# Performance work log

Measured on AMD Instinct MI355X. Metric: run time of the kernel, lower is better.

## Reference

```python
import jax, jax.numpy as jnp
import numpy as np

IN_F, OUT_F = 4096, 16384
B, S = 4, 2048
SCALE = 0.02

def setup_inputs() -> dict:
    key = jax.random.key(0)
    k1, k2 = jax.random.split(key)
    x = jax.random.normal(k1, (B, S, IN_F), dtype=jnp.float32)
    # ternary weights in {-1, 0, +1}
    weight_ternary = jax.random.randint(k2, (OUT_F, IN_F), -1, 2, dtype=jnp.int32)
    weight_scale = jnp.full((1,), SCALE, dtype=jnp.float32)
    return {"x": x, "weight_ternary": weight_ternary, "weight_scale": weight_scale}

def reference(x, weight_ternary, weight_scale):
    # dequantize ternary weight
    w = weight_ternary.astype(jnp.float32) * weight_scale  # [OUT_F, IN_F]
    # per-token int8 activation quant/dequant
    x_scale = jnp.clip(jnp.max(jnp.abs(x), axis=-1, keepdims=True), 1e-5, None)
    x_quant = jnp.round(jnp.clip(x / x_scale * 127.0, -128.0, 127.0))
    x_final = x_quant * x_scale / 127.0
    # linear: x_final @ w.T
    return jnp.einsum('bsi,oi->bso', x_final, w)
```

## Files before the change

kernel.cpp:

```cpp
#include <hip/hip_runtime.h>

#define IN_F 4096
#define OUT_F 16384
#define MTOK 8192

#define BM 256
#define BN 256
#define BK 64
#define NKT (IN_F / BK)

typedef __attribute__((ext_vector_type(4)))  int   i32x4;
typedef __attribute__((ext_vector_type(4)))  float f32x4;

__device__ __forceinline__ void gload_lds16(const void* g, void* l) {
    __builtin_amdgcn_global_load_lds(
        (const __attribute__((address_space(1))) void*)g,
        (__attribute__((address_space(3))) void*)l,
        16, 0, 0);
}

__global__ __launch_bounds__(256) void k_quant(const float* __restrict__ x,
                                               char* __restrict__ xq,
                                               float* __restrict__ xs) {
    const int m = blockIdx.x;
    const int t = threadIdx.x;
    const float* xrow = x + (size_t)m * IN_F;

    f32x4 v[4];
    float mx = 0.f;
#pragma unroll
    for (int i = 0; i < 4; ++i) {
        v[i] = *(const f32x4*)&xrow[(i * 256 + t) * 4];
        mx = fmaxf(mx, fmaxf(fmaxf(fabsf(v[i].x), fabsf(v[i].y)),
                             fmaxf(fabsf(v[i].z), fabsf(v[i].w))));
    }
#pragma unroll
    for (int off = 32; off > 0; off >>= 1)
        mx = fmaxf(mx, __shfl_xor(mx, off));

    __shared__ float wmax[4];
    const int wid = t >> 6;
    if ((t & 63) == 0) wmax[wid] = mx;
    __syncthreads();
    const float scale = fmaxf(fmaxf(fmaxf(wmax[0], wmax[1]),
                                    fmaxf(wmax[2], wmax[3])), 1e-5f);
    const float inv = 127.0f / scale;

    int* xqi = (int*)(xq + (size_t)m * IN_F);
#pragma unroll
    for (int i = 0; i < 4; ++i) {
        int q0 = (int)rintf(fminf(fmaxf(v[i].x * inv, -128.f), 127.f));
        int q1 = (int)rintf(fminf(fmaxf(v[i].y * inv, -128.f), 127.f));
        int q2 = (int)rintf(fminf(fmaxf(v[i].z * inv, -128.f), 127.f));
        int q3 = (int)rintf(fminf(fmaxf(v[i].w * inv, -128.f), 127.f));
        xqi[i * 256 + t] = (q0 & 255) | ((q1 & 255) << 8) |
                           ((q2 & 255) << 16) | (q3 << 24);
    }
    if (t == 0) xs[m] = scale;
}

__global__ __launch_bounds__(256) void k_wconv(const int* __restrict__ wt,
                                               int* __restrict__ w8) {
    const int total4 = OUT_F * IN_F / 4;
    int idx = blockIdx.x * 256 + threadIdx.x;
    const int stride = gridDim.x * 256;
    for (; idx < total4; idx += stride) {
        i32x4 w = *(const i32x4*)&wt[(size_t)idx * 4];
        w8[idx] = (w.x & 255) | ((w.y & 255) << 8) |
                  ((w.z & 255) << 16) | (w.w << 24);
    }
}

__global__ __launch_bounds__(512, 2) void k_gemm(
    const char*  __restrict__ Aq,
    const char*  __restrict__ Bq,
    const float* __restrict__ xs,
    const float* __restrict__ wsp,
    float*       __restrict__ C) {
    __shared__ __align__(16) char lds[98304];

    const int t    = threadIdx.x;
    const int lane = t & 63;
    const int wid  = t >> 6;
    const int wr   = wid >> 2;
    const int wc   = wid & 3;

    const int bid = blockIdx.x;
    const int bn  = (bid & 7) * 8 + ((bid >> 3) & 7);
    const int bm  = bid >> 6;
    const int mBase = bm * BM;
    const int nBase = bn * BN;

    const int r0 = t >> 2;
    const int c0 = (((t & 3) ^ ((t >> 3) & 3)) << 4);

#define STAGE(kt, bx) do {                                                     \
        const size_t ks = (size_t)(kt) * BK;                                   \
        gload_lds16(Aq + (size_t)(mBase + r0) * IN_F + ks + c0,                \
                    lds + (bx) * 16384 + wid * 1024);                          \
        gload_lds16(Aq + (size_t)(mBase + 128 + r0) * IN_F + ks + c0,          \
                    lds + (bx) * 16384 + 8192 + wid * 1024);                   \
        gload_lds16(Bq + (size_t)(nBase + r0) * IN_F + ks + c0,                \
                    lds + 49152 + (bx) * 16384 + wid * 1024);                  \
        gload_lds16(Bq + (size_t)(nBase + 128 + r0) * IN_F + ks + c0,          \
                    lds + 49152 + (bx) * 16384 + 8192 + wid * 1024);           \
    } while (0)

    const int fOff = (lane & 15) * 64 + ((((lane >> 4) ^ (lane >> 1)) & 3) << 4);
    const char* ldsA = lds + wr * 8192;
    const char* ldsB = lds + 49152 + wc * 4096;

#define BAR()   __builtin_amdgcn_s_barrier()
#define VM4()   asm volatile("s_waitcnt vmcnt(4)" ::: "memory")
#define VM0()   asm volatile("s_waitcnt vmcnt(0)" ::: "memory")

    i32x4 acc[8][4];
#pragma unroll
    for (int i = 0; i < 8; ++i)
#pragma unroll
        for (int j = 0; j < 4; ++j)
            acc[i][j] = (i32x4){0, 0, 0, 0};

    STAGE(0, 0);
    STAGE(1, 1);
    VM4();
    BAR();

    int x = 0, x2 = 2;
    for (int kt = 0; kt < NKT; ++kt) {
        const int xo = x * 16384;
        const bool more = (kt + 2 < NKT);

        i32x4 b[4], a[8];
#pragma unroll
        for (int ni = 0; ni < 4; ++ni)
            b[ni] = *(const i32x4*)(ldsB + xo + ni * 1024 + fOff);
#pragma unroll
        for (int mi = 0; mi < 8; ++mi)
            a[mi] = *(const i32x4*)(ldsA + xo + mi * 1024 + fOff);

        if (more) STAGE(kt + 2, x2);

        __builtin_amdgcn_s_setprio(1);
#pragma unroll
        for (int mi = 0; mi < 8; ++mi)
#pragma unroll
            for (int ni = 0; ni < 4; ++ni)
                acc[mi][ni] = __builtin_amdgcn_mfma_i32_16x16x64_i8(
                    a[mi], b[ni], acc[mi][ni], 0, 0, 0);
        __builtin_amdgcn_s_setprio(0);

        if (more) { VM4(); } else { VM0(); }
        BAR();

        x  = (x  == 2) ? 0 : x  + 1;
        x2 = (x2 == 2) ? 0 : x2 + 1;
    }

    const float wsc = wsp[0] * (1.0f / 127.0f);
#pragma unroll
    for (int mi = 0; mi < 8; ++mi) {
        float rs[4];
#pragma unroll
        for (int r = 0; r < 4; ++r)
            rs[r] = xs[mBase + wr * 128 + mi * 16 + (lane >> 4) * 4 + r] * wsc;
#pragma unroll
        for (int ni = 0; ni < 4; ++ni) {
            const int col = nBase + wc * 64 + ni * 16 + (lane & 15);
#pragma unroll
            for (int r = 0; r < 4; ++r) {
                const int row = mBase + wr * 128 + mi * 16 + (lane >> 4) * 4 + r;
                C[(size_t)row * OUT_F + col] = (float)acc[mi][ni][r] * rs[r];
            }
        }
    }
}

extern "C" void kernel_launch(void* const* d_in, const int* in_sizes, int n_in,
                              void* d_out, int out_size, void* d_ws, size_t ws_size,
                              hipStream_t stream) {
    const float* x   = (const float*)d_in[0];
    const int*   wt  = (const int*)d_in[1];
    const float* wsp = (const float*)d_in[2];
    float* out = (float*)d_out;

    char*  w8 = (char*)d_ws;
    char*  xq = (char*)d_ws + (size_t)OUT_F * IN_F;
    float* xs = (float*)((char*)d_ws + (size_t)OUT_F * IN_F
                                     + (size_t)MTOK * IN_F);

    k_wconv<<<8192, 256, 0, stream>>>(wt, (int*)w8);
    k_quant<<<MTOK, 256, 0, stream>>>(x, xq, xs);

    const int grid = (MTOK / BM) * (OUT_F / BN);
    k_gemm<<<grid, 512, 0, stream>>>(xq, w8, xs, wsp, out);
}
```

Measured before the change: 644.0 us.

## Load B fragments directly from global into registers, halving LDS usage

The weight (B) tile no longer goes through LDS. Each wave loads its B MFMA fragments straight from global memory into registers, double-buffered one k-step ahead, while A still uses the 3-stage LDS pipeline. LDS drops from 96KB to 48KB, which could allow more occupancy and removes the LDS reads for B. In exchange, B reuse across the two row-waves now happens in cache rather than LDS, so global traffic rises, and the loop is unrolled by two with a peeled tail and adjusted vmcnt waits.

Result: slower. 906.8 us (+40.8%).

```diff
diff --git a/kernel.cpp b/kernel.cpp
--- a/kernel.cpp
+++ b/kernel.cpp
@@ -77,7 +77,7 @@
     const float* __restrict__ xs,
     const float* __restrict__ wsp,
     float*       __restrict__ C) {
-    __shared__ __align__(16) char lds[98304];
+    __shared__ __align__(16) char lds[49152];
 
     const int t    = threadIdx.x;
     const int lane = t & 63;
@@ -100,19 +100,37 @@
                     lds + (bx) * 16384 + wid * 1024);                          \
         gload_lds16(Aq + (size_t)(mBase + 128 + r0) * IN_F + ks + c0,          \
                     lds + (bx) * 16384 + 8192 + wid * 1024);                   \
-        gload_lds16(Bq + (size_t)(nBase + r0) * IN_F + ks + c0,                \
-                    lds + 49152 + (bx) * 16384 + wid * 1024);                  \
-        gload_lds16(Bq + (size_t)(nBase + 128 + r0) * IN_F + ks + c0,          \
-                    lds + 49152 + (bx) * 16384 + 8192 + wid * 1024);           \
     } while (0)
 
     const int fOff = (lane & 15) * 64 + ((((lane >> 4) ^ (lane >> 1)) & 3) << 4);
     const char* ldsA = lds + wr * 8192;
-    const char* ldsB = lds + 49152 + wc * 4096;
+
+    const char* bBase = Bq + (size_t)(nBase + wc * 64 + (lane & 15)) * IN_F
+                           + ((lane >> 4) << 4);
+
+#define LOADB(dst, kt)                                                         \
+    _Pragma("unroll")                                                          \
+    for (int ni = 0; ni < 4; ++ni)                                             \
+        dst[ni] = *(const i32x4*)(bBase + ni * 65536 + (size_t)(kt) * BK);
+
+#define RDA(a, XO)                                                             \
+    _Pragma("unroll")                                                          \
+    for (int mi = 0; mi < 8; ++mi)                                             \
+        a[mi] = *(const i32x4*)(ldsA + (XO) + mi * 1024 + fOff);
+
+#define MFMAC(a, b)                                                            \
+    __builtin_amdgcn_s_setprio(1);                                             \
+    _Pragma("unroll")                                                          \
+    for (int mi = 0; mi < 8; ++mi)                                             \
+        _Pragma("unroll")                                                      \
+        for (int ni = 0; ni < 4; ++ni)                                         \
+            acc[mi][ni] = __builtin_amdgcn_mfma_i32_16x16x64_i8(               \
+                a[mi], b[ni], acc[mi][ni], 0, 0, 0);                           \
+    __builtin_amdgcn_s_setprio(0);
 
 #define BAR()   __builtin_amdgcn_s_barrier()
+#define VM6()   asm volatile("s_waitcnt vmcnt(6)" ::: "memory")
 #define VM4()   asm volatile("s_waitcnt vmcnt(4)" ::: "memory")
-#define VM0()   asm volatile("s_waitcnt vmcnt(0)" ::: "memory")
 
     i32x4 acc[8][4];
 #pragma unroll
@@ -121,40 +139,45 @@
         for (int j = 0; j < 4; ++j)
             acc[i][j] = (i32x4){0, 0, 0, 0};
 
+    i32x4 bA[4], bB[4];
+
     STAGE(0, 0);
     STAGE(1, 1);
-    VM4();
+    LOADB(bA, 0);
+    VM6();
     BAR();
 
     int x = 0, x2 = 2;
-    for (int kt = 0; kt < NKT; ++kt) {
-        const int xo = x * 16384;
-        const bool more = (kt + 2 < NKT);
-
-        i32x4 b[4], a[8];
-#pragma unroll
-        for (int ni = 0; ni < 4; ++ni)
-            b[ni] = *(const i32x4*)(ldsB + xo + ni * 1024 + fOff);
-#pragma unroll
-        for (int mi = 0; mi < 8; ++mi)
-            a[mi] = *(const i32x4*)(ldsA + xo + mi * 1024 + fOff);
-
-        if (more) STAGE(kt + 2, x2);
-
-        __builtin_amdgcn_s_setprio(1);
-#pragma unroll
-        for (int mi = 0; mi < 8; ++mi)
-#pragma unroll
-            for (int ni = 0; ni < 4; ++ni)
-                acc[mi][ni] = __builtin_amdgcn_mfma_i32_16x16x64_i8(
-                    a[mi], b[ni], acc[mi][ni], 0, 0, 0);
-        __builtin_amdgcn_s_setprio(0);
-
-        if (more) { VM4(); } else { VM0(); }
+#define GBODY(kt, BU, BL) do {                                                 \
+        LOADB(BL, (kt) + 1);                                                   \
+        i32x4 a[8];                                                            \
+        RDA(a, x * 16384);                                                     \
+        STAGE((kt) + 2, x2);                                                   \
+        MFMAC(a, BU);                                                          \
+        VM6();                                                                 \
+        BAR();                                                                 \
+        x  = (x  == 2) ? 0 : x  + 1;                                           \
+        x2 = (x2 == 2) ? 0 : x2 + 1;                                           \
+    } while (0)
+
+    for (int it = 0; it < 31; ++it) {
+        const int k0 = 2 * it;
+        GBODY(k0,     bA, bB);
+        GBODY(k0 + 1, bB, bA);
+    }
+
+    {
+        LOADB(bB, 63);
+        i32x4 a[8];
+        RDA(a, x * 16384);
+        MFMAC(a, bA);
+        VM4();
         BAR();
-
-        x  = (x  == 2) ? 0 : x  + 1;
-        x2 = (x2 == 2) ? 0 : x2 + 1;
+    }
+    {
+        i32x4 a[8];
+        RDA(a, 0);
+        MFMAC(a, bB);
     }
 
     const float wsc = wsp[0] * (1.0f / 127.0f);
```

## Merge preprocessing kernels and interleave LDS fragment loads with MFMA quadrants

Applied to the files above, without the earlier changes.

The weight conversion and activation quantization kernels become one launch, with the block index choosing the branch, so one launch gap goes away and the two memory-bound phases can overlap. In the GEMM main loop, fragment loads are split into A/B halves and issued between four groups of MFMAs, so LDS reads overlap matrix math instead of all loading up front. This may cut register pressure from holding all fragments at once. It relies on the compiler keeping the interleaved order, and the merged kernel now has a larger grid mixing two kinds of work.

Result: no change. 644.0 us (+0.0%).

```diff
diff --git a/kernel.cpp b/kernel.cpp
--- a/kernel.cpp
+++ b/kernel.cpp
@@ -19,55 +19,56 @@
         16, 0, 0);
 }
 
-__global__ __launch_bounds__(256) void k_quant(const float* __restrict__ x,
-                                               char* __restrict__ xq,
-                                               float* __restrict__ xs) {
-    const int m = blockIdx.x;
+__global__ __launch_bounds__(256) void k_pre(const float* __restrict__ x,
+                                             const int*   __restrict__ wt,
+                                             char*  __restrict__ xq,
+                                             float* __restrict__ xs,
+                                             int*   __restrict__ w8) {
     const int t = threadIdx.x;
-    const float* xrow = x + (size_t)m * IN_F;
-
-    f32x4 v[4];
-    float mx = 0.f;
-#pragma unroll
-    for (int i = 0; i < 4; ++i) {
-        v[i] = *(const f32x4*)&xrow[(i * 256 + t) * 4];
-        mx = fmaxf(mx, fmaxf(fmaxf(fabsf(v[i].x), fabsf(v[i].y)),
-                             fmaxf(fabsf(v[i].z), fabsf(v[i].w))));
-    }
-#pragma unroll
-    for (int off = 32; off > 0; off >>= 1)
-        mx = fmaxf(mx, __shfl_xor(mx, off));
-
-    __shared__ float wmax[4];
-    const int wid = t >> 6;
-    if ((t & 63) == 0) wmax[wid] = mx;
-    __syncthreads();
-    const float scale = fmaxf(fmaxf(fmaxf(wmax[0], wmax[1]),
-                                    fmaxf(wmax[2], wmax[3])), 1e-5f);
-    const float inv = 127.0f / scale;
-
-    int* xqi = (int*)(xq + (size_t)m * IN_F);
-#pragma unroll
-    for (int i = 0; i < 4; ++i) {
-        int q0 = (int)rintf(fminf(fmaxf(v[i].x * inv, -128.f), 127.f));
-        int q1 = (int)rintf(fminf(fmaxf(v[i].y * inv, -128.f), 127.f));
-        int q2 = (int)rintf(fminf(fmaxf(v[i].z * inv, -128.f), 127.f));
-        int q3 = (int)rintf(fminf(fmaxf(v[i].w * inv, -128.f), 127.f));
-        xqi[i * 256 + t] = (q0 & 255) | ((q1 & 255) << 8) |
-                           ((q2 & 255) << 16) | (q3 << 24);
-    }
-    if (t == 0) xs[m] = scale;
-}
-
-__global__ __launch_bounds__(256) void k_wconv(const int* __restrict__ wt,
-                                               int* __restrict__ w8) {
-    const int total4 = OUT_F * IN_F / 4;
-    int idx = blockIdx.x * 256 + threadIdx.x;
-    const int stride = gridDim.x * 256;
-    for (; idx < total4; idx += stride) {
-        i32x4 w = *(const i32x4*)&wt[(size_t)idx * 4];
-        w8[idx] = (w.x & 255) | ((w.y & 255) << 8) |
-                  ((w.z & 255) << 16) | (w.w << 24);
+    if (blockIdx.x < MTOK) {
+        const int m = blockIdx.x;
+        const float* xrow = x + (size_t)m * IN_F;
+
+        f32x4 v[4];
+        float mx = 0.f;
+#pragma unroll
+        for (int i = 0; i < 4; ++i) {
+            v[i] = *(const f32x4*)&xrow[(i * 256 + t) * 4];
+            mx = fmaxf(mx, fmaxf(fmaxf(fabsf(v[i].x), fabsf(v[i].y)),
+                                 fmaxf(fabsf(v[i].z), fabsf(v[i].w))));
+        }
+#pragma unroll
+        for (int off = 32; off > 0; off >>= 1)
+            mx = fmaxf(mx, __shfl_xor(mx, off));
+
+        __shared__ float wmax[4];
+        const int wid = t >> 6;
+        if ((t & 63) == 0) wmax[wid] = mx;
+        __syncthreads();
+        const float scale = fmaxf(fmaxf(fmaxf(wmax[0], wmax[1]),
+                                        fmaxf(wmax[2], wmax[3])), 1e-5f);
+        const float inv = 127.0f / scale;
+
+        int* xqi = (int*)(xq + (size_t)m * IN_F);
+#pragma unroll
+        for (int i = 0; i < 4; ++i) {
+            int q0 = (int)rintf(fminf(fmaxf(v[i].x * inv, -128.f), 127.f));
+            int q1 = (int)rintf(fminf(fmaxf(v[i].y * inv, -128.f), 127.f));
+            int q2 = (int)rintf(fminf(fmaxf(v[i].z * inv, -128.f), 127.f));
+            int q3 = (int)rintf(fminf(fmaxf(v[i].w * inv, -128.f), 127.f));
+            xqi[i * 256 + t] = (q0 & 255) | ((q1 & 255) << 8) |
+                               ((q2 & 255) << 16) | (q3 << 24);
+        }
+        if (t == 0) xs[m] = scale;
+    } else {
+        const int total4 = OUT_F * IN_F / 4;
+        int idx = (blockIdx.x - MTOK) * 256 + t;
+        const int stride = 8192 * 256;
+        for (; idx < total4; idx += stride) {
+            i32x4 w = *(const i32x4*)&wt[(size_t)idx * 4];
+            w8[idx] = (w.x & 255) | ((w.y & 255) << 8) |
+                      ((w.z & 255) << 16) | (w.w << 24);
+        }
     }
 }
 
@@ -110,6 +111,17 @@
     const char* ldsA = lds + wr * 8192;
     const char* ldsB = lds + 49152 + wc * 4096;
 
+#define MFMA8(Af, AB, Bf, BB, NIB)                                             \
+    __builtin_amdgcn_s_setprio(1);                                             \
+    _Pragma("unroll")                                                          \
+    for (int mi = 0; mi < 4; ++mi)                                             \
+        _Pragma("unroll")                                                      \
+        for (int ni = 0; ni < 2; ++ni)                                         \
+            acc[(AB) + mi][(NIB) + ni] =                                       \
+                __builtin_amdgcn_mfma_i32_16x16x64_i8(                         \
+                    Af[mi], Bf[ni], acc[(AB) + mi][(NIB) + ni], 0, 0, 0);      \
+    __builtin_amdgcn_s_setprio(0);
+
 #define BAR()   __builtin_amdgcn_s_barrier()
 #define VM4()   asm volatile("s_waitcnt vmcnt(4)" ::: "memory")
 #define VM0()   asm volatile("s_waitcnt vmcnt(0)" ::: "memory")
@@ -130,26 +142,28 @@
     for (int kt = 0; kt < NKT; ++kt) {
         const int xo = x * 16384;
         const bool more = (kt + 2 < NKT);
-
-        i32x4 b[4], a[8];
-#pragma unroll
-        for (int ni = 0; ni < 4; ++ni)
-            b[ni] = *(const i32x4*)(ldsB + xo + ni * 1024 + fOff);
-#pragma unroll
-        for (int mi = 0; mi < 8; ++mi)
-            a[mi] = *(const i32x4*)(ldsA + xo + mi * 1024 + fOff);
-
+        i32x4 aLo[4], aHi[4], bLo[2], bHi[2];
+
+#pragma unroll
+        for (int mi = 0; mi < 4; ++mi)
+            aLo[mi] = *(const i32x4*)(ldsA + xo + mi * 1024 + fOff);
+#pragma unroll
+        for (int ni = 0; ni < 2; ++ni)
+            bLo[ni] = *(const i32x4*)(ldsB + xo + ni * 1024 + fOff);
+        MFMA8(aLo, 0, bLo, 0, 0);
+
+#pragma unroll
+        for (int ni = 0; ni < 2; ++ni)
+            bHi[ni] = *(const i32x4*)(ldsB + xo + (2 + ni) * 1024 + fOff);
+        MFMA8(aLo, 0, bHi, 0, 2);
+
+#pragma unroll
+        for (int mi = 0; mi < 4; ++mi)
+            aHi[mi] = *(const i32x4*)(ldsA + xo + (4 + mi) * 1024 + fOff);
         if (more) STAGE(kt + 2, x2);
-
-        __builtin_amdgcn_s_setprio(1);
-#pragma unroll
-        for (int mi = 0; mi < 8; ++mi)
-#pragma unroll
-            for (int ni = 0; ni < 4; ++ni)
-                acc[mi][ni] = __builtin_amdgcn_mfma_i32_16x16x64_i8(
-                    a[mi], b[ni], acc[mi][ni], 0, 0, 0);
-        __builtin_amdgcn_s_setprio(0);
-
+        MFMA8(aHi, 4, bHi, 0, 2);
+
+        MFMA8(aHi, 4, bLo, 0, 0);
         if (more) { VM4(); } else { VM0(); }
         BAR();
 
@@ -189,8 +203,7 @@
     float* xs = (float*)((char*)d_ws + (size_t)OUT_F * IN_F
                                      + (size_t)MTOK * IN_F);
 
-    k_wconv<<<8192, 256, 0, stream>>>(wt, (int*)w8);
-    k_quant<<<MTOK, 256, 0, stream>>>(x, xq, xs);
+    k_pre<<<MTOK + 8192, 256, 0, stream>>>(x, wt, xq, xs, (int*)w8);
 
     const int grid = (MTOK / BM) * (OUT_F / BN);
     k_gemm<<<grid, 512, 0, stream>>>(xq, w8, xs, wsp, out);
```

## Enlarge per-wave GEMM tile to 128x128 with 4-stage LDS and fragment double-buffering

Applied to the files above, without the earlier changes.

The GEMM block shrinks to 4 waves, each computing a 128x128 output tile instead of 128x64. This roughly halves LDS fragment reads per MFMA. LDS grows to a 4-stage ring of 128 KB, and the loop is unrolled by four so the next k-step's A/B fragments load into a second register set while the current MFMAs run. The cost is heavy register pressure: 256 accumulator registers plus 128 fragment registers, with launch bounds set to 1 block. Occupancy drops to one 4-wave block per CU, so latency hiding relies entirely on the software pipeline.

New measurement: 1.061 ms. 1.65x slower.

```diff
diff --git a/kernel.cpp b/kernel.cpp
--- a/kernel.cpp
+++ b/kernel.cpp
@@ -71,19 +71,19 @@
     }
 }
 
-__global__ __launch_bounds__(512, 2) void k_gemm(
+__global__ __launch_bounds__(256, 1) void k_gemm(
     const char*  __restrict__ Aq,
     const char*  __restrict__ Bq,
     const float* __restrict__ xs,
     const float* __restrict__ wsp,
     float*       __restrict__ C) {
-    __shared__ __align__(16) char lds[98304];
+    __shared__ __align__(16) char lds[131072];
 
     const int t    = threadIdx.x;
     const int lane = t & 63;
     const int wid  = t >> 6;
-    const int wr   = wid >> 2;
-    const int wc   = wid & 3;
+    const int wr   = wid >> 1;
+    const int wc   = wid & 1;
 
     const int bid = blockIdx.x;
     const int bn  = (bid & 7) * 8 + ((bid >> 3) & 7);
@@ -96,65 +96,75 @@
 
 #define STAGE(kt, bx) do {                                                     \
         const size_t ks = (size_t)(kt) * BK;                                   \
-        gload_lds16(Aq + (size_t)(mBase + r0) * IN_F + ks + c0,                \
-                    lds + (bx) * 16384 + wid * 1024);                          \
-        gload_lds16(Aq + (size_t)(mBase + 128 + r0) * IN_F + ks + c0,          \
-                    lds + (bx) * 16384 + 8192 + wid * 1024);                   \
-        gload_lds16(Bq + (size_t)(nBase + r0) * IN_F + ks + c0,                \
-                    lds + 49152 + (bx) * 16384 + wid * 1024);                  \
-        gload_lds16(Bq + (size_t)(nBase + 128 + r0) * IN_F + ks + c0,          \
-                    lds + 49152 + (bx) * 16384 + 8192 + wid * 1024);           \
+        const char* Ab = Aq + (size_t)(mBase + r0) * IN_F + ks + c0;           \
+        const char* Bb = Bq + (size_t)(nBase + r0) * IN_F + ks + c0;           \
+        char* dA = lds + (bx) * 16384 + wid * 1024;                            \
+        char* dB = lds + 65536 + (bx) * 16384 + wid * 1024;                    \
+        gload_lds16(Ab,                       dA);                             \
+        gload_lds16(Ab + (size_t) 64 * IN_F,  dA + 4096);                      \
+        gload_lds16(Ab + (size_t)128 * IN_F,  dA + 8192);                      \
+        gload_lds16(Ab + (size_t)192 * IN_F,  dA + 12288);                     \
+        gload_lds16(Bb,                       dB);                             \
+        gload_lds16(Bb + (size_t) 64 * IN_F,  dB + 4096);                      \
+        gload_lds16(Bb + (size_t)128 * IN_F,  dB + 8192);                      \
+        gload_lds16(Bb + (size_t)192 * IN_F,  dB + 12288);                     \
     } while (0)
 
     const int fOff = (lane & 15) * 64 + ((((lane >> 4) ^ (lane >> 1)) & 3) << 4);
-    const char* ldsA = lds + wr * 8192;
-    const char* ldsB = lds + 49152 + wc * 4096;
-
-#define BAR()   __builtin_amdgcn_s_barrier()
-#define VM4()   asm volatile("s_waitcnt vmcnt(4)" ::: "memory")
+
+#define RD(av, bv, bx) do {                                                    \
+        const char* pA = lds + (bx) * 16384 + wr * 8192;                       \
+        const char* pB = lds + 65536 + (bx) * 16384 + wc * 8192;               \
+        _Pragma("unroll")                                                      \
+        for (int i = 0; i < 8; ++i)                                            \
+            av[i] = *(const i32x4*)(pA + i * 1024 + fOff);                     \
+        _Pragma("unroll")                                                      \
+        for (int i = 0; i < 8; ++i)                                            \
+            bv[i] = *(const i32x4*)(pB + i * 1024 + fOff);                     \
+    } while (0)
+
+#define M64(av, bv)                                                            \
+    __builtin_amdgcn_s_setprio(1);                                             \
+    _Pragma("unroll")                                                          \
+    for (int mi = 0; mi < 8; ++mi)                                             \
+        _Pragma("unroll")                                                      \
+        for (int ni = 0; ni < 8; ++ni)                                         \
+            acc[mi][ni] = __builtin_amdgcn_mfma_i32_16x16x64_i8(               \
+                av[mi], bv[ni], acc[mi][ni], 0, 0, 0);                         \
+    __builtin_amdgcn_s_setprio(0);
+
+#define BARM()  asm volatile("s_barrier" ::: "memory")
+#define VM8()   asm volatile("s_waitcnt vmcnt(8)" ::: "memory")
 #define VM0()   asm volatile("s_waitcnt vmcnt(0)" ::: "memory")
 
-    i32x4 acc[8][4];
+#define BODY(kt, CA, CB, NA, NB, BX2, BXN) do {                                \
+        if ((kt) + 2 < NKT) { STAGE((kt) + 2, BX2); VM8(); }                   \
+        else if ((kt) + 1 < NKT) { VM0(); }                                    \
+        if ((kt) + 1 < NKT) { BARM(); RD(NA, NB, BXN); }                       \
+        M64(CA, CB);                                                           \
+    } while (0)
+
+    i32x4 acc[8][8];
 #pragma unroll
     for (int i = 0; i < 8; ++i)
 #pragma unroll
-        for (int j = 0; j < 4; ++j)
+        for (int j = 0; j < 8; ++j)
             acc[i][j] = (i32x4){0, 0, 0, 0};
+
+    i32x4 a0[8], b0[8], a1[8], b1[8];
 
     STAGE(0, 0);
     STAGE(1, 1);
-    VM4();
-    BAR();
-
-    int x = 0, x2 = 2;
-    for (int kt = 0; kt < NKT; ++kt) {
-        const int xo = x * 16384;
-        const bool more = (kt + 2 < NKT);
-
-        i32x4 b[4], a[8];
-#pragma unroll
-        for (int ni = 0; ni < 4; ++ni)
-            b[ni] = *(const i32x4*)(ldsB + xo + ni * 1024 + fOff);
-#pragma unroll
-        for (int mi = 0; mi < 8; ++mi)
-            a[mi] = *(const i32x4*)(ldsA + xo + mi * 1024 + fOff);
-
-        if (more) STAGE(kt + 2, x2);
-
-        __builtin_amdgcn_s_setprio(1);
-#pragma unroll
-        for (int mi = 0; mi < 8; ++mi)
-#pragma unroll
-            for (int ni = 0; ni < 4; ++ni)
-                acc[mi][ni] = __builtin_amdgcn_mfma_i32_16x16x64_i8(
-                    a[mi], b[ni], acc[mi][ni], 0, 0, 0);
-        __builtin_amdgcn_s_setprio(0);
-
-        if (more) { VM4(); } else { VM0(); }
-        BAR();
-
-        x  = (x  == 2) ? 0 : x  + 1;
-        x2 = (x2 == 2) ? 0 : x2 + 1;
+    VM8();
+    BARM();
+    RD(a0, b0, 0);
+
+    for (int it = 0; it < NKT / 4; ++it) {
+        const int k0 = it * 4;
+        BODY(k0 + 0, a0, b0, a1, b1, 2, 1);
+        BODY(k0 + 1, a1, b1, a0, b0, 3, 2);
+        BODY(k0 + 2, a0, b0, a1, b1, 0, 3);
+        BODY(k0 + 3, a1, b1, a0, b0, 1, 0);
     }
 
     const float wsc = wsp[0] * (1.0f / 127.0f);
@@ -165,8 +175,8 @@
         for (int r = 0; r < 4; ++r)
             rs[r] = xs[mBase + wr * 128 + mi * 16 + (lane >> 4) * 4 + r] * wsc;
 #pragma unroll
-        for (int ni = 0; ni < 4; ++ni) {
-            const int col = nBase + wc * 64 + ni * 16 + (lane & 15);
+        for (int ni = 0; ni < 8; ++ni) {
+            const int col = nBase + wc * 128 + ni * 16 + (lane & 15);
 #pragma unroll
             for (int r = 0; r < 4; ++r) {
                 const int row = mBase + wr * 128 + mi * 16 + (lane >> 4) * 4 + r;
@@ -193,5 +203,5 @@
     k_quant<<<MTOK, 256, 0, stream>>>(x, xq, xs);
 
     const int grid = (MTOK / BM) * (OUT_F / BN);
-    k_gemm<<<grid, 512, 0, stream>>>(xq, w8, xs, wsp, out);
-}
+    k_gemm<<<grid, 256, 0, stream>>>(xq, w8, xs, wsp, out);
+}
```
